# Kernel optimization log

Measured on AMD Instinct MI355X. Metric: run time of the kernel, lower is better.

The kernel has to match this reference:

```python
import jax, jax.numpy as jnp
import numpy as np

N = 50000   # nodes
E = 800000  # edges (avg degree 16)
D = 128     # node latent dim
DE = 128    # edge latent dim
L = 3       # num_mp_steps


def setup_inputs() -> dict:
    key = jax.random.key(0)
    ks = jax.random.split(key, 10)
    s = 0.05
    return dict(
        x=jax.random.normal(ks[0], (N, D), jnp.float32),
        edge_index=jax.random.randint(ks[1], (2, E), 0, N, jnp.int32),
        edge_attr=jax.random.normal(ks[2], (E, DE), jnp.float32),
        # per-layer GATConv params (stacked over L layers)
        W=jax.random.normal(ks[3], (L, D, D), jnp.float32) * s,        # lin (shared src/dst)
        att_src=jax.random.normal(ks[4], (L, D), jnp.float32) * s,
        att_dst=jax.random.normal(ks[5], (L, D), jnp.float32) * s,
        W_e=jax.random.normal(ks[6], (L, DE, D), jnp.float32) * s,     # lin_edge
        att_edge=jax.random.normal(ks[7], (L, D), jnp.float32) * s,
        bias=jnp.zeros((L, D), jnp.float32),
        ln_gamma=jnp.ones((L, D), jnp.float32),                        # post-conv LayerNorm
        ln_beta=jnp.zeros((L, D), jnp.float32),
    )


def reference(x, edge_index, edge_attr, W, att_src, att_dst, W_e, att_edge, bias, ln_gamma, ln_beta):
    n = x.shape[0]
    src, dst = edge_index[0], edge_index[1]

    # add_self_loops with fill_value='mean': self-loop edge feature of node i is
    # the mean of raw edge features of edges incoming to i (0 if none).
    ones = jnp.ones((src.shape[0],), x.dtype)
    deg = jax.ops.segment_sum(ones, dst, num_segments=n)
    loop_attr = jax.ops.segment_sum(edge_attr, dst, num_segments=n) / jnp.maximum(deg, 1.0)[:, None]
    loop = jnp.arange(n, dtype=src.dtype)
    src_f = jnp.concatenate([src, loop])            # [E+N]
    dst_f = jnp.concatenate([dst, loop])            # [E+N]
    ea_f = jnp.concatenate([edge_attr, loop_attr], axis=0)  # [E+N, DE]

    def layer(h_in, p):
        Wl, asl, adl, Wel, ael, bl, gl, bel = p
        h = h_in @ Wl                                              # [N, D]
        # per-edge attention logits (heads=1)
        a = (h @ asl)[src_f] + (h @ adl)[dst_f] + ea_f @ (Wel @ ael)  # [E+N]
        a = jnp.where(a > 0, a, 0.2 * a)                           # LeakyReLU(0.2)
        # segment softmax over destination nodes (every node has a self loop)
        m = jax.ops.segment_max(a, dst_f, num_segments=n)
        ea = jnp.exp(a - m[dst_f])
        denom = jax.ops.segment_sum(ea, dst_f, num_segments=n)
        alpha = ea / denom[dst_f]
        out = jax.ops.segment_sum(h[src_f] * alpha[:, None], dst_f, num_segments=n) + bl
        # LayerNorm (elementwise affine)
        mu = jnp.mean(out, axis=-1, keepdims=True)
        var = jnp.var(out, axis=-1, keepdims=True)
        out = (out - mu) * jax.lax.rsqrt(var + 1e-5) * gl + bel
        return out, None

    h, _ = jax.lax.scan(layer, x, (W, att_src, att_dst, W_e, att_edge, bias, ln_gamma, ln_beta))
    return h
```

## Files before the change

kernel.cpp:

```cpp
#include <hip/hip_runtime.h>
#include <cstdint>

#define D 128
#define LNUM 3

typedef short short8 __attribute__((ext_vector_type(8)));
typedef float f32x4 __attribute__((ext_vector_type(4)));

static __device__ __forceinline__ float wred_sum(float x) {
#pragma unroll
    for (int off = 32; off; off >>= 1) x += __shfl_xor(x, off);
    return x;
}
static __device__ __forceinline__ float wred_max(float x) {
#pragma unroll
    for (int off = 32; off; off >>= 1) x = fmaxf(x, __shfl_xor(x, off));
    return x;
}
static __device__ __forceinline__ uint32_t f2bf_rne(float x) {
    uint32_t u = __float_as_uint(x);
    uint32_t r = u + 0x7fffu + ((u >> 16) & 1u);
    return r >> 16;
}


__global__ __launch_bounds__(256) void pre_k(const float* __restrict__ W, const float* __restrict__ We,
                                             const float* __restrict__ ae, const float* __restrict__ x,
                                             const int* __restrict__ dst,
                                             uint16_t* __restrict__ Wt, float* __restrict__ vbuf,
                                             uint16_t* __restrict__ xb, int* __restrict__ cnt,
                                             int ND4, int E) {
    int tid = blockIdx.x * 256 + threadIdx.x;
    int stride = gridDim.x * 256;
    for (int i = tid; i < ND4; i += stride) {
        float4 v = *(const float4*)&x[(size_t)i * 4];
        uint2 o;
        o.x = f2bf_rne(v.x) | (f2bf_rne(v.y) << 16);
        o.y = f2bf_rne(v.z) | (f2bf_rne(v.w) << 16);
        *(uint2*)&xb[(size_t)i * 4] = o;
    }
    for (int e = tid; e < E; e += stride) atomicAdd(&cnt[dst[e]], 1);
    for (int i = tid; i < LNUM * D * D; i += stride) {
        int l = i >> 14;
        int r = i & (D * D - 1);
        int j = r >> 7, k = r & 127;
        Wt[i] = (uint16_t)f2bf_rne(W[(size_t)l * D * D + (size_t)k * D + j]);
    }
    if (tid < LNUM * D) {
        int l = tid >> 7, j = tid & 127;
        const float* Wrow = We + ((size_t)l * D + j) * D;
        const float* a = ae + (size_t)l * D;
        float s = 0.f;
        for (int d = 0; d < D; ++d) s += Wrow[d] * a[d];
        vbuf[tid] = s;
    }
}


__global__ __launch_bounds__(1024) void scan_k(const int* __restrict__ cnt, int* __restrict__ rowptr, int N) {
    __shared__ int sh[1024];
    int t = threadIdx.x;
    int chunk = (N + 1023) >> 10;
    int b = t * chunk;
    int e = min(b + chunk, N);
    int s = 0;
    for (int i = b; i < e; ++i) s += cnt[i];
    sh[t] = s;
    __syncthreads();
    for (int off = 1; off < 1024; off <<= 1) {
        int v = (t >= off) ? sh[t - off] : 0;
        __syncthreads();
        sh[t] += v;
        __syncthreads();
    }
    int run = sh[t] - s;
    for (int i = b; i < e; ++i) { rowptr[i] = run; run += cnt[i]; }
    if (t == 1023) rowptr[N] = sh[1023];
}


__global__ __launch_bounds__(256) void fillec_k(const float* __restrict__ ea, const float* __restrict__ vbuf,
                                                const int* __restrict__ src, const int* __restrict__ dst,
                                                const int* __restrict__ rowptr, int* __restrict__ cnt,
                                                uint4* __restrict__ rec, int E) {
    __shared__ float vs[3][D];
    int t = threadIdx.x;
    if (t < D) {
        vs[0][t] = vbuf[t];
        vs[1][t] = vbuf[D + t];
        vs[2][t] = vbuf[2 * D + t];
    }
    __syncthreads();
    int e = blockIdx.x * 32 + (t >> 3);
    int sub = t & 7;
    if (e >= E) return;
    const float* row = ea + (size_t)e * D + sub * 16;
    float p0 = 0.f, p1 = 0.f, p2 = 0.f;
#pragma unroll
    for (int i = 0; i < 4; ++i) {
        float4 v = *(const float4*)&row[i * 4];
        int c = sub * 16 + i * 4;
        p0 += v.x * vs[0][c] + v.y * vs[0][c + 1] + v.z * vs[0][c + 2] + v.w * vs[0][c + 3];
        p1 += v.x * vs[1][c] + v.y * vs[1][c + 1] + v.z * vs[1][c + 2] + v.w * vs[1][c + 3];
        p2 += v.x * vs[2][c] + v.y * vs[2][c + 1] + v.z * vs[2][c + 2] + v.w * vs[2][c + 3];
    }
#pragma unroll
    for (int off = 1; off < 8; off <<= 1) {
        p0 += __shfl_xor(p0, off);
        p1 += __shfl_xor(p1, off);
        p2 += __shfl_xor(p2, off);
    }
    if (sub == 0) {
        int d = dst[e];
        int p = atomicSub(&cnt[d], 1) - 1;
        int q = rowptr[d] + p;
        uint4 r;
        r.x = (uint32_t)src[e];
        r.y = __float_as_uint(p0);
        r.z = __float_as_uint(p1);
        r.w = __float_as_uint(p2);
        rec[q] = r;
    }
}


__global__ __launch_bounds__(256) void gemm_mfma_k(const uint16_t* __restrict__ A,
                                                   const uint16_t* __restrict__ Wt,
                                                   const float* __restrict__ as_,
                                                   const float* __restrict__ ad_,
                                                   uint16_t* __restrict__ hbf,
                                                   float* __restrict__ hs, float* __restrict__ hd, int N) {
    __shared__ uint4 As[64 * 16];
    int t = threadIdx.x;
    int row0 = blockIdx.x * 64;
#pragma unroll
    for (int it = 0; it < 4; ++it) {
        int idx = it * 256 + t;
        int r = idx >> 4, s = idx & 15;
        int gr = row0 + r;
        uint4 v = make_uint4(0u, 0u, 0u, 0u);
        if (gr < N) v = *(const uint4*)&A[(size_t)gr * D + s * 8];
        As[r * 16 + (s ^ (r & 7))] = v;
    }
    __syncthreads();
    int w = t >> 6, l = t & 63;
    int lrow = l & 15, lk = l >> 4;
    int rbase = w * 16;
    short8 afrag[4];
#pragma unroll
    for (int ks = 0; ks < 4; ++ks) {
        int r = rbase + lrow;
        int s = (ks * 4 + lk) ^ (r & 7);
        afrag[ks] = __builtin_bit_cast(short8, As[r * 16 + s]);
    }
    float psum[4] = {0.f, 0.f, 0.f, 0.f}, pdum[4] = {0.f, 0.f, 0.f, 0.f};
#pragma unroll
    for (int ct = 0; ct < 8; ++ct) {
        f32x4 acc = {0.f, 0.f, 0.f, 0.f};
#pragma unroll
        for (int ks = 0; ks < 4; ++ks) {
            short8 b = *(const short8*)&Wt[(size_t)(ct * 16 + lrow) * D + ks * 32 + lk * 8];
            acc = __builtin_amdgcn_mfma_f32_16x16x32_bf16(afrag[ks], b, acc, 0, 0, 0);
        }
        int col_g = ct * 16 + lrow;
        float av = as_[col_g], dv = ad_[col_g];
#pragma unroll
        for (int r = 0; r < 4; ++r) {
            float v = acc[r];
            psum[r] += v * av;
            pdum[r] += v * dv;
            int row_g = row0 + rbase + lk * 4 + r;
            if (row_g < N) hbf[(size_t)row_g * D + col_g] = (uint16_t)f2bf_rne(v);
        }
    }
#pragma unroll
    for (int r = 0; r < 4; ++r) {
        float ps = psum[r], pd = pdum[r];
#pragma unroll
        for (int off = 1; off < 16; off <<= 1) {
            ps += __shfl_xor(ps, off);
            pd += __shfl_xor(pd, off);
        }
        if (lrow == 0) {
            int row_g = row0 + rbase + lk * 4 + r;
            if (row_g < N) { hs[row_g] = ps; hd[row_g] = pd; }
        }
    }
}


__global__ __launch_bounds__(256) void node_k(const uint32_t* __restrict__ hb, const float* __restrict__ hs,
                                              const float* __restrict__ hd, const uint4* __restrict__ rec,
                                              const int* __restrict__ rowptr,
                                              const float* __restrict__ bias, const float* __restrict__ gamma,
                                              const float* __restrict__ beta,
                                              uint32_t* __restrict__ outb, float* __restrict__ outf,
                                              int N, int lsel) {
    __shared__ float s_al[4][66];
    __shared__ int s_co[4][66];
    int w = threadIdx.x >> 6;
    int lane = threadIdx.x & 63;
    int wid = blockIdx.x * 4 + w;
    if (wid >= N) return;
    int beg = rowptr[wid], end = rowptr[wid + 1];
    int deg = end - beg;
    float hdi = hd[wid];
    float hsi = hs[wid];
    float acc0 = 0.f, acc1 = 0.f;

    if (deg <= 63) {
        bool v = lane < deg;
        uint4 r = v ? rec[beg + lane] : make_uint4(0u, 0u, 0u, 0u);
        int col = (int)r.x;
        uint32_t ecu = lsel == 0 ? r.y : (lsel == 1 ? r.z : r.w);
        float ec = __uint_as_float(ecu);
        float a = v ? (hs[col] + hdi + ec) : -3e38f;
        a = a > 0.f ? a : 0.2f * a;
        float sumec = wred_sum(v ? ec : 0.f);
        float ecs = deg > 0 ? sumec / (float)deg : 0.f;
        float as_ = hsi + hdi + ecs;
        as_ = as_ > 0.f ? as_ : 0.2f * as_;
        float m = fmaxf(wred_max(a), as_);
        float p = __expf(a - m);
        float ps = __expf(as_ - m);
        float denom = wred_sum(p) + ps;
        float inv = 1.f / denom;
        s_al[w][lane] = p * inv;
        s_co[w][lane] = col;
        if (lane == 0) { s_al[w][deg] = ps * inv; s_co[w][deg] = wid; }
        __asm__ volatile("s_waitcnt lgkmcnt(0)" ::: "memory");
        int ne = deg + 1;
        int j = 0;
        for (; j + 4 <= ne; j += 4) {
            int c0 = s_co[w][j], c1 = s_co[w][j + 1], c2 = s_co[w][j + 2], c3 = s_co[w][j + 3];
            float a0 = s_al[w][j], a1 = s_al[w][j + 1], a2 = s_al[w][j + 2], a3 = s_al[w][j + 3];
            uint32_t b0 = hb[(size_t)c0 * 64 + lane];
            uint32_t b1 = hb[(size_t)c1 * 64 + lane];
            uint32_t b2 = hb[(size_t)c2 * 64 + lane];
            uint32_t b3 = hb[(size_t)c3 * 64 + lane];
            acc0 += a0 * __uint_as_float(b0 << 16) + a1 * __uint_as_float(b1 << 16) +
                    a2 * __uint_as_float(b2 << 16) + a3 * __uint_as_float(b3 << 16);
            acc1 += a0 * __uint_as_float(b0 & 0xffff0000u) + a1 * __uint_as_float(b1 & 0xffff0000u) +
                    a2 * __uint_as_float(b2 & 0xffff0000u) + a3 * __uint_as_float(b3 & 0xffff0000u);
        }
        for (; j < ne; ++j) {
            int c0 = s_co[w][j];
            float a0 = s_al[w][j];
            uint32_t b0 = hb[(size_t)c0 * 64 + lane];
            acc0 += a0 * __uint_as_float(b0 << 16);
            acc1 += a0 * __uint_as_float(b0 & 0xffff0000u);
        }
    } else {
        float m = -3e38f, dsum = 0.f, sumec = 0.f;
        for (int base = 0; base < deg; base += 64) {
            int jj = base + lane;
            bool v = jj < deg;
            uint4 r = v ? rec[beg + jj] : make_uint4(0u, 0u, 0u, 0u);
            uint32_t ecu = lsel == 0 ? r.y : (lsel == 1 ? r.z : r.w);
            float ec = __uint_as_float(ecu);
            float a = v ? (hs[(int)r.x] + hdi + ec) : -3e38f;
            a = a > 0.f ? a : 0.2f * a;
            sumec += wred_sum(v ? ec : 0.f);
            float cm = wred_max(a);
            float nm = fmaxf(m, cm);
            dsum = dsum * __expf(m - nm) + wred_sum(__expf(a - nm));
            m = nm;
        }
        float ecs = sumec / (float)deg;
        float as_ = hsi + hdi + ecs;
        as_ = as_ > 0.f ? as_ : 0.2f * as_;
        float nm = fmaxf(m, as_);
        dsum = dsum * __expf(m - nm) + __expf(as_ - nm);
        m = nm;
        float inv = 1.f / dsum;
        for (int base = 0; base < deg; base += 64) {
            int jj = base + lane;
            bool v = jj < deg;
            uint4 r = v ? rec[beg + jj] : make_uint4(0u, 0u, 0u, 0u);
            int col = (int)r.x;
            uint32_t ecu = lsel == 0 ? r.y : (lsel == 1 ? r.z : r.w);
            float ec = __uint_as_float(ecu);
            float a = v ? (hs[col] + hdi + ec) : -3e38f;
            a = a > 0.f ? a : 0.2f * a;
            __asm__ volatile("s_waitcnt lgkmcnt(0)" ::: "memory");
            s_al[w][lane] = __expf(a - m) * inv;
            s_co[w][lane] = col;
            __asm__ volatile("s_waitcnt lgkmcnt(0)" ::: "memory");
            int cnt = min(64, deg - base);
            for (int k = 0; k < cnt; ++k) {
                int c = s_co[w][k];
                float al = s_al[w][k];
                uint32_t b = hb[(size_t)c * 64 + lane];
                acc0 += al * __uint_as_float(b << 16);
                acc1 += al * __uint_as_float(b & 0xffff0000u);
            }
        }
        float alS = __expf(as_ - m) * inv;
        uint32_t b = hb[(size_t)wid * 64 + lane];
        acc0 += alS * __uint_as_float(b << 16);
        acc1 += alS * __uint_as_float(b & 0xffff0000u);
    }

    float2 bi = *(const float2*)&bias[lane * 2];
    float o0 = acc0 + bi.x, o1 = acc1 + bi.y;
    float mean = wred_sum(o0 + o1) * (1.f / 128.f);
    float d0 = o0 - mean, d1 = o1 - mean;
    float var = wred_sum(d0 * d0 + d1 * d1) * (1.f / 128.f);
    float rstd = rsqrtf(var + 1e-5f);
    float2 g = *(const float2*)&gamma[lane * 2];
    float2 be = *(const float2*)&beta[lane * 2];
    float2 o;
    o.x = d0 * rstd * g.x + be.x;
    o.y = d1 * rstd * g.y + be.y;
    if (outf) {
        *(float2*)&outf[(size_t)wid * D + lane * 2] = o;
    } else {
        outb[(size_t)wid * 64 + lane] = f2bf_rne(o.x) | (f2bf_rne(o.y) << 16);
    }
}


extern "C" void kernel_launch(void* const* d_in, const int* in_sizes, int n_in,
                              void* d_out, int out_size, void* d_ws, size_t ws_size,
                              hipStream_t stream) {
    const float* x = (const float*)d_in[0];
    const int* ei = (const int*)d_in[1];
    const float* ea = (const float*)d_in[2];
    const float* W = (const float*)d_in[3];
    const float* att_src = (const float*)d_in[4];
    const float* att_dst = (const float*)d_in[5];
    const float* We = (const float*)d_in[6];
    const float* att_edge = (const float*)d_in[7];
    const float* bias = (const float*)d_in[8];
    const float* gamma = (const float*)d_in[9];
    const float* beta = (const float*)d_in[10];

    int N = in_sizes[0] / D;
    int E = in_sizes[1] / 2;
    const int* srcA = ei;
    const int* dstA = ei + E;

    float* p = (float*)d_ws;
    float* hsb = p;   p += N;
    float* hdb = p;   p += N;
    float* vbuf = p;  p += LNUM * D;
    uint16_t* xb = (uint16_t*)p;
    uint16_t* hbf = xb + (size_t)N * D;
    uint16_t* hnb = hbf + (size_t)N * D;
    uint16_t* Wt = hnb + (size_t)N * D;
    uint4* rec = (uint4*)(Wt + (size_t)LNUM * D * D);
    int* ip = (int*)(rec + E);
    int* rowptr = ip; ip += N + 1;
    int* cnt = ip;    ip += N;

    hipMemsetAsync(cnt, 0, sizeof(int) * N, stream);
    pre_k<<<1536, 256, 0, stream>>>(W, We, att_edge, x, dstA, Wt, vbuf, xb, cnt, N * D / 4, E);
    scan_k<<<1, 1024, 0, stream>>>(cnt, rowptr, N);
    fillec_k<<<(E + 31) / 32, 256, 0, stream>>>(ea, vbuf, srcA, dstA, rowptr, cnt, rec, E);

    const uint16_t* hin = xb;
    for (int l = 0; l < LNUM; ++l) {
        gemm_mfma_k<<<(N + 63) / 64, 256, 0, stream>>>(hin, Wt + (size_t)l * D * D,
                                                       att_src + (size_t)l * D, att_dst + (size_t)l * D,
                                                       hbf, hsb, hdb, N);
        bool last = (l == LNUM - 1);
        node_k<<<(N + 3) / 4, 256, 0, stream>>>((const uint32_t*)hbf, hsb, hdb, rec, rowptr,
                                                bias + (size_t)l * D, gamma + (size_t)l * D,
                                                beta + (size_t)l * D,
                                                last ? nullptr : (uint32_t*)hnb,
                                                last ? (float*)d_out : nullptr, N, l);
        hin = hnb;
    }
}
```

Baseline: 431.4 us.

## Split edge permutation from edge-coefficient pass, index records indirectly

Edge records are now written in original edge order, with no scattered writes. A separate set of blocks in the same launch builds a CSR permutation index with atomics. The node kernel reads each edge's record through that index on every layer, which adds an extra dependent random gather of 16-byte records across all three layers. The aim is to decouple the atomic counting from the streaming edge-attribute reduction, at the cost of more indirect reads in the hot aggregation kernel.

```diff
diff --git a/kernel.cpp b/kernel.cpp
--- a/kernel.cpp
+++ b/kernel.cpp
@@ -79,19 +79,28 @@
 }
 
 
-__global__ __launch_bounds__(256) void fillec_k(const float* __restrict__ ea, const float* __restrict__ vbuf,
+__global__ __launch_bounds__(256) void ecperm_k(const float* __restrict__ ea, const float* __restrict__ vbuf,
                                                 const int* __restrict__ src, const int* __restrict__ dst,
                                                 const int* __restrict__ rowptr, int* __restrict__ cnt,
-                                                uint4* __restrict__ rec, int E) {
+                                                uint4* __restrict__ rec0, int* __restrict__ idx,
+                                                int E, int PERM_BLOCKS) {
+    int t = threadIdx.x;
+    if ((int)blockIdx.x < PERM_BLOCKS) {
+        int e = blockIdx.x * 256 + t;
+        if (e >= E) return;
+        int d = dst[e];
+        int p = atomicSub(&cnt[d], 1) - 1;
+        idx[rowptr[d] + p] = e;
+        return;
+    }
     __shared__ float vs[3][D];
-    int t = threadIdx.x;
     if (t < D) {
         vs[0][t] = vbuf[t];
         vs[1][t] = vbuf[D + t];
         vs[2][t] = vbuf[2 * D + t];
     }
     __syncthreads();
-    int e = blockIdx.x * 32 + (t >> 3);
+    int e = (blockIdx.x - PERM_BLOCKS) * 32 + (t >> 3);
     int sub = t & 7;
     if (e >= E) return;
     const float* row = ea + (size_t)e * D + sub * 16;
@@ -111,15 +120,12 @@
         p2 += __shfl_xor(p2, off);
     }
     if (sub == 0) {
-        int d = dst[e];
-        int p = atomicSub(&cnt[d], 1) - 1;
-        int q = rowptr[d] + p;
         uint4 r;
         r.x = (uint32_t)src[e];
         r.y = __float_as_uint(p0);
         r.z = __float_as_uint(p1);
         r.w = __float_as_uint(p2);
-        rec[q] = r;
+        rec0[e] = r;
     }
 }
 
@@ -135,8 +141,8 @@
     int row0 = blockIdx.x * 64;
 #pragma unroll
     for (int it = 0; it < 4; ++it) {
-        int idx = it * 256 + t;
-        int r = idx >> 4, s = idx & 15;
+        int idx2 = it * 256 + t;
+        int r = idx2 >> 4, s = idx2 & 15;
         int gr = row0 + r;
         uint4 v = make_uint4(0u, 0u, 0u, 0u);
         if (gr < N) v = *(const uint4*)&A[(size_t)gr * D + s * 8];
@@ -190,8 +196,8 @@
 
 
 __global__ __launch_bounds__(256) void node_k(const uint32_t* __restrict__ hb, const float* __restrict__ hs,
-                                              const float* __restrict__ hd, const uint4* __restrict__ rec,
-                                              const int* __restrict__ rowptr,
+                                              const float* __restrict__ hd, const uint4* __restrict__ rec0,
+                                              const int* __restrict__ idx, const int* __restrict__ rowptr,
                                               const float* __restrict__ bias, const float* __restrict__ gamma,
                                               const float* __restrict__ beta,
                                               uint32_t* __restrict__ outb, float* __restrict__ outf,
@@ -210,7 +216,8 @@
 
     if (deg <= 63) {
         bool v = lane < deg;
-        uint4 r = v ? rec[beg + lane] : make_uint4(0u, 0u, 0u, 0u);
+        int e = v ? idx[beg + lane] : 0;
+        uint4 r = v ? rec0[e] : make_uint4(0u, 0u, 0u, 0u);
         int col = (int)r.x;
         uint32_t ecu = lsel == 0 ? r.y : (lsel == 1 ? r.z : r.w);
         float ec = __uint_as_float(ecu);
@@ -255,7 +262,8 @@
         for (int base = 0; base < deg; base += 64) {
             int jj = base + lane;
             bool v = jj < deg;
-            uint4 r = v ? rec[beg + jj] : make_uint4(0u, 0u, 0u, 0u);
+            int e = v ? idx[beg + jj] : 0;
+            uint4 r = v ? rec0[e] : make_uint4(0u, 0u, 0u, 0u);
             uint32_t ecu = lsel == 0 ? r.y : (lsel == 1 ? r.z : r.w);
             float ec = __uint_as_float(ecu);
             float a = v ? (hs[(int)r.x] + hdi + ec) : -3e38f;
@@ -276,7 +284,8 @@
         for (int base = 0; base < deg; base += 64) {
             int jj = base + lane;
             bool v = jj < deg;
-            uint4 r = v ? rec[beg + jj] : make_uint4(0u, 0u, 0u, 0u);
+            int e = v ? idx[beg + jj] : 0;
+            uint4 r = v ? rec0[e] : make_uint4(0u, 0u, 0u, 0u);
             int col = (int)r.x;
             uint32_t ecu = lsel == 0 ? r.y : (lsel == 1 ? r.z : r.w);
             float ec = __uint_as_float(ecu);
@@ -343,20 +352,25 @@
     float* p = (float*)d_ws;
     float* hsb = p;   p += N;
     float* hdb = p;   p += N;
-    float* vbuf = p;  p += LNUM * D;
+    float* vbuf = p;  p += LNUM * D + 128;
     uint16_t* xb = (uint16_t*)p;
     uint16_t* hbf = xb + (size_t)N * D;
     uint16_t* hnb = hbf + (size_t)N * D;
     uint16_t* Wt = hnb + (size_t)N * D;
-    uint4* rec = (uint4*)(Wt + (size_t)LNUM * D * D);
-    int* ip = (int*)(rec + E);
+    uint4* rec0 = (uint4*)(Wt + (size_t)LNUM * D * D);
+    int* ip = (int*)(rec0 + E);
+    int* idx = ip;    ip += E;
     int* rowptr = ip; ip += N + 1;
     int* cnt = ip;    ip += N;
+
+    int PERM_BLOCKS = (E + 255) / 256;
+    int EC_BLOCKS = (E + 31) / 32;
 
     hipMemsetAsync(cnt, 0, sizeof(int) * N, stream);
     pre_k<<<1536, 256, 0, stream>>>(W, We, att_edge, x, dstA, Wt, vbuf, xb, cnt, N * D / 4, E);
     scan_k<<<1, 1024, 0, stream>>>(cnt, rowptr, N);
-    fillec_k<<<(E + 31) / 32, 256, 0, stream>>>(ea, vbuf, srcA, dstA, rowptr, cnt, rec, E);
+    ecperm_k<<<PERM_BLOCKS + EC_BLOCKS, 256, 0, stream>>>(ea, vbuf, srcA, dstA, rowptr, cnt,
+                                                          rec0, idx, E, PERM_BLOCKS);
 
     const uint16_t* hin = xb;
     for (int l = 0; l < LNUM; ++l) {
@@ -364,7 +378,7 @@
                                                        att_src + (size_t)l * D, att_dst + (size_t)l * D,
                                                        hbf, hsb, hdb, N);
         bool last = (l == LNUM - 1);
-        node_k<<<(N + 3) / 4, 256, 0, stream>>>((const uint32_t*)hbf, hsb, hdb, rec, rowptr,
+        node_k<<<(N + 3) / 4, 256, 0, stream>>>((const uint32_t*)hbf, hsb, hdb, rec0, idx, rowptr,
                                                 bias + (size_t)l * D, gamma + (size_t)l * D,
                                                 beta + (size_t)l * D,
                                                 last ? nullptr : (uint32_t*)hnb,
```

After: 486.3 us. +12.7%, slower.
